# Kernel tuning notes

Hardware: AMD Instinct MI355X
Metric: run time of the kernel (lower is better)

Reference implementation:

```python
import jax, jax.numpy as jnp
import numpy as np

QN, QP = -8.0, 7.0  # int4 quantization range used by the cutlass q4 kernel
SCALE_DENOM = 11.269  # ~sqrt(127), from set_activation_scale


def _quant4(t, clip):
    # clip-based dynamic quantization to int4 grid (values kept in float)
    return jnp.clip(jnp.round(t / clip), QN, QP)


def setup_inputs() -> dict:
    key = jax.random.key(0)
    kx, ky = jax.random.split(key)
    x = jax.random.normal(kx, (4, 16, 1024, 256), dtype=jnp.float32)
    y = jax.random.normal(ky, (4, 16, 256, 1024), dtype=jnp.float32)
    # set_activation_scale: alpha = 2 * |t|.mean() / 11.269 (module uses x for both)
    x_clip = 2.0 * jnp.mean(jnp.abs(x)) / SCALE_DENOM
    y_clip = 2.0 * jnp.mean(jnp.abs(x)) / SCALE_DENOM
    return {"x": x, "y": y, "x_clip": x_clip, "y_clip": y_clip}


def reference(x, y, x_clip, y_clip):
    # quantize both operands to int4 grid, integer-grid matmul, dequant by clip scales
    qx = _quant4(x, x_clip)  # [B, H, M, K]
    qy = _quant4(y, y_clip)  # [B, H, K, N]
    out = jnp.einsum("bhmk,bhkn->bhmn", qx, qy)
    return out * x_clip * y_clip
```

## Files before the change

### kernel.cpp

```cpp
#include <hip/hip_runtime.h>

#define NBATCH 64
#define M_DIM  1024
#define K_DIM  256
#define N_DIM  1024

typedef __attribute__((ext_vector_type(4)))  int   i32x4;
typedef __attribute__((ext_vector_type(4)))  float f32x4;

union Pack16 { char c[16]; i32x4 i; };

__device__ __forceinline__ float quant4f(float v, float clip) {
    return fminf(fmaxf(rintf(v / clip), -8.0f), 7.0f);
}

__global__ __launch_bounds__(256) void quant_kernel(
        const float* __restrict__ x, const float* __restrict__ y,
        const float* __restrict__ xclip_p, const float* __restrict__ yclip_p,
        char* __restrict__ qx, char* __restrict__ qyT) {
    __shared__ float tile[64][65];
    const int bid = blockIdx.x;
    const int tid = threadIdx.x;

    if (bid < 4096) {
        const float clip = xclip_p[0];
        const int idx = (bid * 256 + tid) * 16;
        Pack16 o;
#pragma unroll
        for (int c = 0; c < 4; ++c) {
            f32x4 v = *(const f32x4*)(x + idx + c * 4);
#pragma unroll
            for (int j = 0; j < 4; ++j)
                o.c[c * 4 + j] = (char)(int)quant4f(v[j], clip);
        }
        *(i32x4*)(qx + idx) = o.i;
    } else {
        const float clip = yclip_p[0];
        const int b2 = bid - 4096;
        const int n0 = (b2 & 15) * 64;
        const int k0 = ((b2 >> 4) & 3) * 64;
        const int b  = b2 >> 6;
        const float* yb = y + (size_t)b * K_DIM * N_DIM;
        const int kl = tid >> 4;
        const int nq = (tid & 15) * 4;
#pragma unroll
        for (int i = 0; i < 4; ++i) {
            f32x4 v = *(const f32x4*)(yb + (size_t)(k0 + kl + i * 16) * N_DIM + n0 + nq);
#pragma unroll
            for (int j = 0; j < 4; ++j)
                tile[kl + i * 16][nq + j] = quant4f(v[j], clip);
        }
        __syncthreads();
        char* ob = qyT + (size_t)b * N_DIM * K_DIM;
        const int nl = tid >> 2;
        const int kc = (tid & 3) * 16;
        Pack16 o;
#pragma unroll
        for (int j = 0; j < 16; ++j)
            o.c[j] = (char)(int)tile[kc + j][nl];
        *(i32x4*)(ob + (size_t)(n0 + nl) * K_DIM + k0 + kc) = o.i;
    }
}

#define GLD16(gp, lp) __builtin_amdgcn_global_load_lds(                         \
    (const __attribute__((address_space(1))) void*)(gp),                        \
    (__attribute__((address_space(3))) void*)(lp), 16, 0, 0)

__global__ __launch_bounds__(256) void q4_gemm_kernel(
        const char* __restrict__ qx,
        const char* __restrict__ qyT,
        const float* __restrict__ xclip_p, const float* __restrict__ yclip_p,
        float* __restrict__ out) {
    const int p = blockIdx.x;
    const int l = (p & 7) * 512 + (p >> 3);
    const int b  = l >> 6;
    const int t  = l & 63;
    const int br = t >> 3;
    const int bc = t & 7;

    __shared__ __align__(16) char smem[16896];
    char* As = smem;
    char* Bs = smem + 8192;
    float (*Cst)[132] = (float (*)[132])smem;

    const int tid  = threadIdx.x;
    const int lane = tid & 63;
    const int wid  = tid >> 6;
    const int wr   = wid >> 1;
    const int wc   = wid & 1;

    const char* Abase = qx  + (size_t)b * M_DIM * K_DIM + (size_t)br * 128 * K_DIM;
    const char* Bbase = qyT + (size_t)b * N_DIM * K_DIM + (size_t)bc * 128 * K_DIM;

    i32x4 acc[4][4] = {};

    const int lrow15 = lane & 15;
    const int s      = lane >> 4;

#pragma unroll
    for (int kt = 0; kt < K_DIM / 64; ++kt) {
        const int k0 = kt * 64;
#pragma unroll
        for (int c = 0; c < 2; ++c) {
            int chunk = tid + c * 256;
            int row   = chunk >> 2;
            int slot  = chunk & 3;
            int ksrc  = ((slot ^ (row & 3)) * 16);
            GLD16(Abase + (size_t)row * K_DIM + k0 + ksrc, As + chunk * 16);
            GLD16(Bbase + (size_t)row * K_DIM + k0 + ksrc, Bs + chunk * 16);
        }
        __syncthreads();

        i32x4 af[4], bf[4];
#pragma unroll
        for (int m = 0; m < 4; ++m) {
            int row = wr * 64 + m * 16 + lrow15;
            af[m] = *(const i32x4*)(As + row * 64 + ((s ^ (row & 3)) * 16));
        }
#pragma unroll
        for (int n = 0; n < 4; ++n) {
            int row = wc * 64 + n * 16 + lrow15;
            bf[n] = *(const i32x4*)(Bs + row * 64 + ((s ^ (row & 3)) * 16));
        }
#pragma unroll
        for (int m = 0; m < 4; ++m)
#pragma unroll
            for (int n = 0; n < 4; ++n)
                acc[m][n] = __builtin_amdgcn_mfma_i32_16x16x64_i8(
                                af[m], bf[n], acc[m][n], 0, 0, 0);
        __syncthreads();
    }

    const float scale = xclip_p[0] * yclip_p[0];
    const size_t cb = (size_t)b * M_DIM * N_DIM
                    + (size_t)(br * 128) * N_DIM + bc * 128;
    const int rsub = (lane >> 4) * 4;
    const int rdr  = tid >> 3;
    const int cdw0 = (tid & 7) * 4;

#pragma unroll
    for (int m = 0; m < 4; ++m) {
#pragma unroll
        for (int n = 0; n < 4; ++n)
#pragma unroll
            for (int j = 0; j < 4; ++j)
                Cst[wr * 16 + rsub + j][wc * 64 + n * 16 + lrow15] =
                    (float)acc[m][n][j] * scale;
        __syncthreads();
        const int grow = (rdr >> 4) * 64 + m * 16 + (rdr & 15);
#pragma unroll
        for (int i = 0; i < 4; ++i) {
            f32x4 v = *(const f32x4*)&Cst[rdr][cdw0 + i * 32];
            __builtin_nontemporal_store(
                v, (f32x4*)(out + cb + (size_t)grow * N_DIM + cdw0 + i * 32));
        }
        __syncthreads();
    }
}

extern "C" void kernel_launch(void* const* d_in, const int* in_sizes, int n_in,
                              void* d_out, int out_size, void* d_ws, size_t ws_size,
                              hipStream_t stream) {
    const float* x     = (const float*)d_in[0];
    const float* y     = (const float*)d_in[1];
    const float* xclip = (const float*)d_in[2];
    const float* yclip = (const float*)d_in[3];
    float* out = (float*)d_out;

    char* qx  = (char*)d_ws;
    char* qyT = qx + (size_t)NBATCH * M_DIM * K_DIM;

    quant_kernel<<<8192, 256, 0, stream>>>(x, y, xclip, yclip, qx, qyT);
    q4_gemm_kernel<<<4096, 256, 0, stream>>>(qx, qyT, xclip, yclip, out);
}
```

Measured before the change: 82.94 us.

## Double-buffer LDS tiles in int8 GEMM to overlap global loads with MFMA

```diff
diff --git a/kernel.cpp b/kernel.cpp
--- a/kernel.cpp
+++ b/kernel.cpp
@@ -66,7 +66,7 @@
     (const __attribute__((address_space(1))) void*)(gp),                        \
     (__attribute__((address_space(3))) void*)(lp), 16, 0, 0)
 
-__global__ __launch_bounds__(256) void q4_gemm_kernel(
+__global__ __launch_bounds__(256, 4) void q4_gemm_kernel(
         const char* __restrict__ qx,
         const char* __restrict__ qyT,
         const float* __restrict__ xclip_p, const float* __restrict__ yclip_p,
@@ -78,9 +78,7 @@
     const int br = t >> 3;
     const int bc = t & 7;
 
-    __shared__ __align__(16) char smem[16896];
-    char* As = smem;
-    char* Bs = smem + 8192;
+    __shared__ __align__(16) char smem[32768];
     float (*Cst)[132] = (float (*)[132])smem;
 
     const int tid  = threadIdx.x;
@@ -92,24 +90,39 @@
     const char* Abase = qx  + (size_t)b * M_DIM * K_DIM + (size_t)br * 128 * K_DIM;
     const char* Bbase = qyT + (size_t)b * N_DIM * K_DIM + (size_t)bc * 128 * K_DIM;
 
+    const int row0  = tid >> 2;
+    const int row1  = (tid + 256) >> 2;
+    const int slot  = tid & 3;
+    const int ks0   = (slot ^ (row0 & 3)) * 16;
+    const int ks1   = (slot ^ (row1 & 3)) * 16;
+
     i32x4 acc[4][4] = {};
 
     const int lrow15 = lane & 15;
     const int s      = lane >> 4;
 
+    {
+        char* As = smem; char* Bs = smem + 8192;
+        GLD16(Abase + (size_t)row0 * K_DIM + ks0, As + tid * 16);
+        GLD16(Bbase + (size_t)row0 * K_DIM + ks0, Bs + tid * 16);
+        GLD16(Abase + (size_t)row1 * K_DIM + ks1, As + (tid + 256) * 16);
+        GLD16(Bbase + (size_t)row1 * K_DIM + ks1, Bs + (tid + 256) * 16);
+    }
+    __syncthreads();
+
 #pragma unroll
-    for (int kt = 0; kt < K_DIM / 64; ++kt) {
-        const int k0 = kt * 64;
-#pragma unroll
-        for (int c = 0; c < 2; ++c) {
-            int chunk = tid + c * 256;
-            int row   = chunk >> 2;
-            int slot  = chunk & 3;
-            int ksrc  = ((slot ^ (row & 3)) * 16);
-            GLD16(Abase + (size_t)row * K_DIM + k0 + ksrc, As + chunk * 16);
-            GLD16(Bbase + (size_t)row * K_DIM + k0 + ksrc, Bs + chunk * 16);
+    for (int kt = 0; kt < 4; ++kt) {
+        char* As = smem + (kt & 1) * 16384;
+        char* Bs = As + 8192;
+        if (kt < 3) {
+            const int kn = (kt + 1) * 64;
+            char* An = smem + ((kt + 1) & 1) * 16384;
+            char* Bn = An + 8192;
+            GLD16(Abase + (size_t)row0 * K_DIM + kn + ks0, An + tid * 16);
+            GLD16(Bbase + (size_t)row0 * K_DIM + kn + ks0, Bn + tid * 16);
+            GLD16(Abase + (size_t)row1 * K_DIM + kn + ks1, An + (tid + 256) * 16);
+            GLD16(Bbase + (size_t)row1 * K_DIM + kn + ks1, Bn + (tid + 256) * 16);
         }
-        __syncthreads();
 
         i32x4 af[4], bf[4];
 #pragma unroll
```

Result: faster. 80.22 us (-3.3%).
